# Performance work log

Measured on AMD Instinct MI355X. Metric: run time of the kernel, lower is better.

The kernel has to match this reference:

```python
import jax, jax.numpy as jnp
import numpy as np

N_HEADS = 4
M = 16            # n_points (neighbors kept per voxel)
DIST = 4          # manhattan distance threshold
D_MODEL = 128
D_FFN = 256
D_CHL = 64
GRID = 96         # spatial_shape per axis
LN_EPS = 1e-5
BN_EPS = 1e-3


def setup_inputs() -> dict:
    key = jax.random.key(0)
    ks = jax.random.split(key, 24)
    N = 8192
    w = lambda k, s: jax.random.normal(k, s, jnp.float32) * 0.02
    z = lambda d: jnp.zeros((d,), jnp.float32)
    o = lambda d: jnp.ones((d,), jnp.float32)
    return {
        "features": jax.random.normal(ks[0], (N, D_CHL), jnp.float32),
        "coords": jax.random.randint(ks[1], (N, 3), 0, GRID, jnp.int32),
        "pe_w1": w(ks[2], (3, D_MODEL // 2)), "pe_b1": z(D_MODEL // 2),
        "pe_w2": w(ks[3], (D_MODEL // 2, D_MODEL)), "pe_b2": z(D_MODEL),
        "in_w": w(ks[4], (D_CHL, D_MODEL)), "in_b": z(D_MODEL),
        "q_w": w(ks[5], (D_MODEL, D_MODEL)), "q_b": z(D_MODEL),
        "k_w": w(ks[6], (D_MODEL, D_MODEL)), "k_b": z(D_MODEL),
        "v_w": w(ks[7], (D_MODEL, D_MODEL)), "v_b": z(D_MODEL),
        "o_w": w(ks[8], (D_MODEL, D_MODEL)), "o_b": z(D_MODEL),
        "n1_g": o(D_MODEL), "n1_b": z(D_MODEL),
        "l1_w": w(ks[9], (D_MODEL, D_FFN)), "l1_b": z(D_FFN),
        "l2_w": w(ks[10], (D_FFN, D_MODEL)), "l2_b": z(D_MODEL),
        "n3_g": o(D_MODEL), "n3_b": z(D_MODEL),
        "fu_w": w(ks[11], (D_MODEL + D_CHL, D_CHL)), "fu_b": z(D_CHL),
        "bn_g": o(D_CHL), "bn_b": z(D_CHL),
    }


def _layernorm(x, g, b):
    mu = jnp.mean(x, -1, keepdims=True)
    var = jnp.mean(jnp.square(x - mu), -1, keepdims=True)
    return (x - mu) * jax.lax.rsqrt(var + LN_EPS) * g + b


def reference(features, coords, pe_w1, pe_b1, pe_w2, pe_b2, in_w, in_b,
              q_w, q_b, k_w, k_b, v_w, v_b, o_w, o_b, n1_g, n1_b,
              l1_w, l1_b, l2_w, l2_b, n3_g, n3_b, fu_w, fu_b, bn_g, bn_b):
    N = features.shape[0]
    hd = D_MODEL // N_HEADS
    ci = coords.astype(jnp.float32)
    # input projection + dynamic learnable positional encoding
    src = features @ in_w + in_b
    vc = ci / (GRID - 1.0)
    src = src + (jax.nn.relu(vc @ pe_w1 + pe_b1) @ pe_w2 + pe_b2)
    # pairwise manhattan distances; accumulate per coordinate to avoid [N,N,3]
    dist = jnp.zeros((N, N), jnp.float32)
    for d in range(3):
        dist = dist + jnp.abs(ci[:, d, None] - ci[None, :, d])
    dist = jnp.where(dist <= DIST, dist, jnp.inf)
    neg_top, idx = jax.lax.top_k(-dist, M)          # [N, M]
    valid = neg_top != -jnp.inf
    # gather neighbor features; invalid slots are zero (as in torch)
    nb = jnp.where(valid[:, :, None], src[jnp.where(valid, idx, 0)], 0.0)  # [N,M,D]
    # cross-attention: query is neighbor 0 (self). NOTE: faithful raw .view
    # reshape of [N,M,D] -> [N,H,M,hd] (interleaves neighbor/head axes as torch does)
    q = (nb[:, :1] @ q_w + q_b).reshape(N, N_HEADS, 1, hd)
    k = (nb @ k_w + k_b).reshape(N, N_HEADS, M, hd)
    v = (nb @ v_w + v_b).reshape(N, N_HEADS, M, hd)
    scores = jnp.einsum('nhqd,nhkd->nhqk', q, k) / jnp.sqrt(jnp.float32(D_MODEL))
    attn = jax.nn.softmax(scores, axis=-1)
    head_out = jnp.einsum('nhqk,nhkd->nhqd', attn, v).reshape(N, D_MODEL)
    out = head_out @ o_w + o_b
    tgt = _layernorm(src + out, n1_g, n1_b)
    # FFN
    tgt2 = jax.nn.relu(tgt @ l1_w + l1_b) @ l2_w + l2_b
    tgt = _layernorm(tgt + tgt2, n3_g, n3_b)
    # EnhancedFusion: concat -> linear -> batchnorm (train-mode stats) -> relu
    fused = jnp.concatenate([features, tgt], axis=1) @ fu_w + fu_b
    mu = jnp.mean(fused, 0)
    var = jnp.var(fused, 0)
    fused = (fused - mu) * jax.lax.rsqrt(var + BN_EPS) * bn_g + bn_b
    return jax.nn.relu(fused)
```

## Files before the change

kernel.cpp:

```cpp
#include <hip/hip_runtime.h>

#define DEVFN __device__ __forceinline__

DEVFN float relu(float x) { return x < 0.f ? 0.f : x; }

__global__ __launch_bounds__(256) void ka_pre_cst(
    const float* __restrict__ features, const int* __restrict__ coords,
    const float* __restrict__ pe_w1, const float* __restrict__ pe_b1,
    const float* __restrict__ pe_w2, const float* __restrict__ pe_b2,
    const float* __restrict__ in_w, const float* __restrict__ in_b,
    const float* __restrict__ q_w, const float* __restrict__ k_w,
    const float* __restrict__ v_w,
    float* __restrict__ src,
    float* __restrict__ qs, float* __restrict__ ks, float* __restrict__ vs,
    int* __restrict__ nbr, float* __restrict__ bnAcc, int N)
{
    __shared__ float sF[512];
    __shared__ float sH[512];
    __shared__ float S[1024];
    __shared__ int   sC[24];
    __shared__ int cnt[16];
    __shared__ int lst[16 * 64];
    __shared__ int outL[256];

    const int tid = threadIdx.x;
    const int nSrcBlocks = N / 8;

    if ((int)blockIdx.x >= nSrcBlocks) {
        const int nb = blockIdx.x - nSrcBlocks;
        const int q0 = nb * 16;
        if (nb == 0 && tid < 128) bnAcc[tid] = 0.f;
        if (tid < 16) cnt[tid] = 0;
        outL[tid] = -1;
        __syncthreads();
        int qx[16], qy[16], qz[16];
#pragma unroll
        for (int q = 0; q < 16; ++q) {
            qx[q] = coords[(q0 + q) * 3 + 0];
            qy[q] = coords[(q0 + q) * 3 + 1];
            qz[q] = coords[(q0 + q) * 3 + 2];
        }
        for (int cd = tid; cd < N; cd += 256) {
            int cx = coords[cd * 3 + 0];
            int cy = coords[cd * 3 + 1];
            int cz = coords[cd * 3 + 2];
#pragma unroll
            for (int q = 0; q < 16; ++q) {
                int dx = cx - qx[q]; dx = dx < 0 ? -dx : dx;
                int dy = cy - qy[q]; dy = dy < 0 ? -dy : dy;
                int dz = cz - qz[q]; dz = dz < 0 ? -dz : dz;
                int d = dx + dy + dz;
                if (d <= 4) {
                    int s = atomicAdd(&cnt[q], 1);
                    if (s < 64) lst[q * 64 + s] = (d << 13) | cd;
                }
            }
        }
        __syncthreads();
        {
            const int q = tid >> 4, t = tid & 15;
            int n = cnt[q]; if (n > 64) n = 64;
            for (int e = t; e < n; e += 16) {
                int key = lst[q * 64 + e];
                int rank = 0;
                for (int j = 0; j < n; ++j) rank += (lst[q * 64 + j] < key) ? 1 : 0;
                if (rank < 16) outL[q * 16 + rank] = key & 8191;
            }
        }
        __syncthreads();
        {
            const int q = tid >> 4, t = tid & 15;
            nbr[(q0 + q) * 16 + t] = outL[q * 16 + t];
        }
        return;
    }

    const int r0 = blockIdx.x * 8;
    if (tid < 24) sC[tid] = coords[r0 * 3 + tid];
    for (int i = tid; i < 512; i += 256) sF[i] = features[r0 * 64 + i];
    __syncthreads();
    for (int i = tid; i < 512; i += 256) {
        int r = i >> 6, t = i & 63;
        float v0 = sC[r * 3 + 0] * (1.f / 95.f);
        float v1 = sC[r * 3 + 1] * (1.f / 95.f);
        float v2 = sC[r * 3 + 2] * (1.f / 95.f);
        float h = v0 * pe_w1[t] + v1 * pe_w1[64 + t] + v2 * pe_w1[128 + t] + pe_b1[t];
        sH[i] = relu(h);
    }
    __syncthreads();
    const int c = tid & 127, rh = tid >> 7;
    {
        float acc[4];
        const float base = in_b[c] + pe_b2[c];
#pragma unroll
        for (int r = 0; r < 4; ++r) acc[r] = base;
        for (int j = 0; j < 64; ++j) {
            float w1 = in_w[j * 128 + c];
            float w2 = pe_w2[j * 128 + c];
#pragma unroll
            for (int r = 0; r < 4; ++r) {
                int rr = rh * 4 + r;
                acc[r] += sF[rr * 64 + j] * w1 + sH[rr * 64 + j] * w2;
            }
        }
#pragma unroll
        for (int r = 0; r < 4; ++r) {
            src[(r0 + rh * 4 + r) * 128 + c] = acc[r];
            S[(rh * 4 + r) * 128 + c] = acc[r];
        }
    }
    __syncthreads();
    {
        float aq[4], ak[4], av[4];
#pragma unroll
        for (int r = 0; r < 4; ++r) { aq[r] = 0.f; ak[r] = 0.f; av[r] = 0.f; }
        for (int k4 = 0; k4 < 32; ++k4) {
            float wq0 = q_w[(k4 * 4 + 0) * 128 + c];
            float wq1 = q_w[(k4 * 4 + 1) * 128 + c];
            float wq2 = q_w[(k4 * 4 + 2) * 128 + c];
            float wq3 = q_w[(k4 * 4 + 3) * 128 + c];
            float wk0 = k_w[(k4 * 4 + 0) * 128 + c];
            float wk1 = k_w[(k4 * 4 + 1) * 128 + c];
            float wk2 = k_w[(k4 * 4 + 2) * 128 + c];
            float wk3 = k_w[(k4 * 4 + 3) * 128 + c];
            float wv0 = v_w[(k4 * 4 + 0) * 128 + c];
            float wv1 = v_w[(k4 * 4 + 1) * 128 + c];
            float wv2 = v_w[(k4 * 4 + 2) * 128 + c];
            float wv3 = v_w[(k4 * 4 + 3) * 128 + c];
#pragma unroll
            for (int r = 0; r < 4; ++r) {
                float4 s = *(const float4*)(&S[(rh * 4 + r) * 128 + k4 * 4]);
                aq[r] += s.x * wq0 + s.y * wq1 + s.z * wq2 + s.w * wq3;
                ak[r] += s.x * wk0 + s.y * wk1 + s.z * wk2 + s.w * wk3;
                av[r] += s.x * wv0 + s.y * wv1 + s.z * wv2 + s.w * wv3;
            }
        }
#pragma unroll
        for (int r = 0; r < 4; ++r) {
            qs[(r0 + rh * 4 + r) * 128 + c] = aq[r];
            ks[(r0 + rh * 4 + r) * 128 + c] = ak[r];
            vs[(r0 + rh * 4 + r) * 128 + c] = av[r];
        }
    }
}

DEVFN void ln_rows8(float* Cb, const float* __restrict__ g,
                    const float* __restrict__ b, int tid)
{
    const int r = tid >> 5, l = tid & 31;
    float x[4]; float s = 0.f, s2 = 0.f;
#pragma unroll
    for (int i = 0; i < 4; ++i) {
        x[i] = Cb[r * 128 + l * 4 + i];
        s += x[i]; s2 += x[i] * x[i];
    }
#pragma unroll
    for (int o = 1; o < 32; o <<= 1) { s += __shfl_xor(s, o); s2 += __shfl_xor(s2, o); }
    float mu = s * (1.f / 128.f);
    float var = s2 * (1.f / 128.f) - mu * mu;
    float rstd = rsqrtf(var + 1e-5f);
#pragma unroll
    for (int i = 0; i < 4; ++i) {
        int cc = l * 4 + i;
        Cb[r * 128 + cc] = (x[i] - mu) * rstd * g[cc] + b[cc];
    }
}

__global__ __launch_bounds__(256) void k4_main_cst(
    const float* __restrict__ features, const float* __restrict__ src,
    const float* __restrict__ qs, const float* __restrict__ ks, const float* __restrict__ vs,
    const int* __restrict__ nbr,
    const float* __restrict__ q_b, const float* __restrict__ k_b,
    const float* __restrict__ v_b,
    const float* __restrict__ o_w, const float* __restrict__ o_b,
    const float* __restrict__ n1_g, const float* __restrict__ n1_b,
    const float* __restrict__ l1_w, const float* __restrict__ l1_b,
    const float* __restrict__ l2_w, const float* __restrict__ l2_b,
    const float* __restrict__ n3_g, const float* __restrict__ n3_b,
    const float* __restrict__ fu_w, const float* __restrict__ fu_b,
    float* __restrict__ fused, float* __restrict__ bnSum, float* __restrict__ bnSq)
{
    __shared__ float A[1024];
    __shared__ float Bt[1024];
    __shared__ float C[1024];
    __shared__ float Q[1024];
    __shared__ float H[2048];
    __shared__ float SC[512];
    __shared__ float F[512];
    __shared__ __align__(16) float bK[128], bV[128];
    __shared__ float bQ[128];
    __shared__ int idxL[128];
    const int tid = threadIdx.x;
    const int r0 = blockIdx.x * 8;

    for (int i = tid; i < 1024; i += 256) A[i] = src[r0 * 128 + i];
    for (int i = tid; i < 512; i += 256) F[i] = features[r0 * 64 + i];
    if (tid < 128) {
        idxL[tid] = nbr[r0 * 16 + tid];
        bQ[tid] = q_b[tid]; bK[tid] = k_b[tid]; bV[tid] = v_b[tid];
    }
    __syncthreads();
    for (int i = tid; i < 1024; i += 256) {
        int r = i >> 7, c = i & 127;
        int i0 = idxL[r * 16];
        Q[i] = (i0 < 0 ? 0.f : qs[i0 * 128 + c]) + bQ[c];
    }
    __syncthreads();

    const int ar = tid >> 5, ah = (tid >> 3) & 3, ag = tid & 7;
    {
#pragma unroll
        for (int jj = 0; jj < 2; ++jj) {
            int j = ag + jj * 8;
            int j4 = j >> 2, ch = j & 3;
            int id = idxL[ar * 16 + ah * 4 + j4];
            float s = 0.f;
#pragma unroll
            for (int c4 = 0; c4 < 8; ++c4) {
                float4 qv = *(const float4*)(&Q[ar * 128 + ah * 32 + c4 * 4]);
                float4 kb = *(const float4*)(&bK[ch * 32 + c4 * 4]);
                float4 kv = make_float4(0.f, 0.f, 0.f, 0.f);
                if (id >= 0) kv = *(const float4*)(ks + id * 128 + ch * 32 + c4 * 4);
                s += qv.x * (kv.x + kb.x) + qv.y * (kv.y + kb.y)
                   + qv.z * (kv.z + kb.z) + qv.w * (kv.w + kb.w);
            }
            SC[ar * 64 + ah * 16 + j] = s * 0.08838834764831845f;
        }
    }
    __syncthreads();

    {
        float p[16];
        float mx = -3.4e38f;
#pragma unroll
        for (int j = 0; j < 16; ++j) { p[j] = SC[ar * 64 + ah * 16 + j]; mx = fmaxf(mx, p[j]); }
        float sum = 0.f;
#pragma unroll
        for (int j = 0; j < 16; ++j) { p[j] = __expf(p[j] - mx); sum += p[j]; }
        float inv = 1.f / sum;
        float4 acc = make_float4(0.f, 0.f, 0.f, 0.f);
#pragma unroll
        for (int j = 0; j < 16; ++j) {
            int j4 = j >> 2, ch = j & 3;
            int id = idxL[ar * 16 + ah * 4 + j4];
            float4 vb = *(const float4*)(&bV[ch * 32 + ag * 4]);
            float4 vv = make_float4(0.f, 0.f, 0.f, 0.f);
            if (id >= 0) vv = *(const float4*)(vs + id * 128 + ch * 32 + ag * 4);
            float w = p[j] * inv;
            acc.x += w * (vv.x + vb.x); acc.y += w * (vv.y + vb.y);
            acc.z += w * (vv.z + vb.z); acc.w += w * (vv.w + vb.w);
        }
        *(float4*)(&Bt[ar * 128 + ah * 32 + ag * 4]) = acc;
    }
    __syncthreads();

    {
        const int c = tid & 127, rh = tid >> 7;
        float acc[4];
        const float ob = o_b[c];
#pragma unroll
        for (int r = 0; r < 4; ++r) acc[r] = ob;
        for (int k4 = 0; k4 < 32; ++k4) {
            float w0 = o_w[(k4 * 4 + 0) * 128 + c];
            float w1 = o_w[(k4 * 4 + 1) * 128 + c];
            float w2 = o_w[(k4 * 4 + 2) * 128 + c];
            float w3 = o_w[(k4 * 4 + 3) * 128 + c];
#pragma unroll
            for (int r = 0; r < 4; ++r) {
                float4 t = *(const float4*)(&Bt[(rh * 4 + r) * 128 + k4 * 4]);
                acc[r] += t.x * w0 + t.y * w1 + t.z * w2 + t.w * w3;
            }
        }
#pragma unroll
        for (int r = 0; r < 4; ++r) {
            int row = rh * 4 + r;
            C[row * 128 + c] = A[row * 128 + c] + acc[r];
        }
    }
    __syncthreads();
    ln_rows8(C, n1_g, n1_b, tid);
    __syncthreads();

    {
        const int f = tid;
        float acc[8];
#pragma unroll
        for (int r = 0; r < 8; ++r) acc[r] = 0.f;
        for (int k4 = 0; k4 < 32; ++k4) {
            float w0 = l1_w[(k4 * 4 + 0) * 256 + f];
            float w1 = l1_w[(k4 * 4 + 1) * 256 + f];
            float w2 = l1_w[(k4 * 4 + 2) * 256 + f];
            float w3 = l1_w[(k4 * 4 + 3) * 256 + f];
#pragma unroll
            for (int r = 0; r < 8; ++r) {
                float4 t = *(const float4*)(&C[r * 128 + k4 * 4]);
                acc[r] += t.x * w0 + t.y * w1 + t.z * w2 + t.w * w3;
            }
        }
        const float bb = l1_b[f];
#pragma unroll
        for (int r = 0; r < 8; ++r) H[r * 256 + f] = relu(acc[r] + bb);
    }
    __syncthreads();

    {
        const int c = tid & 127, rh = tid >> 7;
        float acc[4];
        const float lb = l2_b[c];
#pragma unroll
        for (int r = 0; r < 4; ++r) acc[r] = lb;
        for (int k4 = 0; k4 < 64; ++k4) {
            float w0 = l2_w[(k4 * 4 + 0) * 128 + c];
            float w1 = l2_w[(k4 * 4 + 1) * 128 + c];
            float w2 = l2_w[(k4 * 4 + 2) * 128 + c];
            float w3 = l2_w[(k4 * 4 + 3) * 128 + c];
#pragma unroll
            for (int r = 0; r < 4; ++r) {
                float4 t = *(const float4*)(&H[(rh * 4 + r) * 256 + k4 * 4]);
                acc[r] += t.x * w0 + t.y * w1 + t.z * w2 + t.w * w3;
            }
        }
#pragma unroll
        for (int r = 0; r < 4; ++r) {
            int row = rh * 4 + r;
            C[row * 128 + c] += acc[r];
        }
    }
    __syncthreads();
    ln_rows8(C, n3_g, n3_b, tid);
    __syncthreads();

    {
        const int c = tid & 63, rg = tid >> 6;
        float acc[2];
        const float fb = fu_b[c];
#pragma unroll
        for (int r = 0; r < 2; ++r) acc[r] = fb;
        for (int j4 = 0; j4 < 16; ++j4) {
            float w0 = fu_w[(j4 * 4 + 0) * 64 + c];
            float w1 = fu_w[(j4 * 4 + 1) * 64 + c];
            float w2 = fu_w[(j4 * 4 + 2) * 64 + c];
            float w3 = fu_w[(j4 * 4 + 3) * 64 + c];
#pragma unroll
            for (int r = 0; r < 2; ++r) {
                float4 t = *(const float4*)(&F[(rg * 2 + r) * 64 + j4 * 4]);
                acc[r] += t.x * w0 + t.y * w1 + t.z * w2 + t.w * w3;
            }
        }
        for (int j4 = 0; j4 < 32; ++j4) {
            float w0 = fu_w[(64 + j4 * 4 + 0) * 64 + c];
            float w1 = fu_w[(64 + j4 * 4 + 1) * 64 + c];
            float w2 = fu_w[(64 + j4 * 4 + 2) * 64 + c];
            float w3 = fu_w[(64 + j4 * 4 + 3) * 64 + c];
#pragma unroll
            for (int r = 0; r < 2; ++r) {
                float4 t = *(const float4*)(&C[(rg * 2 + r) * 128 + j4 * 4]);
                acc[r] += t.x * w0 + t.y * w1 + t.z * w2 + t.w * w3;
            }
        }
#pragma unroll
        for (int r = 0; r < 2; ++r) {
            int row = rg * 2 + r;
            float v = acc[r];
            fused[(r0 + row) * 64 + c] = v;
            H[row * 64 + c] = v;
        }
    }
    __syncthreads();
    if (tid < 64) {
        float s = 0.f, s2 = 0.f;
#pragma unroll
        for (int r = 0; r < 8; ++r) { float x = H[r * 64 + tid]; s += x; s2 += x * x; }
        atomicAdd(&bnSum[tid], s);
        atomicAdd(&bnSq[tid], s2);
    }
}

__global__ __launch_bounds__(256) void k5_bn_cst(
    const float* __restrict__ fused, const float* __restrict__ bnSum,
    const float* __restrict__ bnSq,
    const float* __restrict__ g, const float* __restrict__ b,
    float* __restrict__ out, int N)
{
    const int total = N * 64;
    const float invN = 1.f / (float)N;
    for (int i = blockIdx.x * 256 + threadIdx.x; i < total; i += gridDim.x * 256) {
        int c = i & 63;
        float mu = bnSum[c] * invN;
        float var = bnSq[c] * invN - mu * mu;
        float x = fused[i];
        float y = (x - mu) * rsqrtf(var + 1e-3f) * g[c] + b[c];
        out[i] = relu(y);
    }
}

extern "C" void kernel_launch(void* const* d_in, const int* in_sizes, int n_in,
                              void* d_out, int out_size, void* d_ws, size_t ws_size,
                              hipStream_t stream)
{
    const float* features = (const float*)d_in[0];
    const int*   coords   = (const int*)d_in[1];
    const float* pe_w1 = (const float*)d_in[2];
    const float* pe_b1 = (const float*)d_in[3];
    const float* pe_w2 = (const float*)d_in[4];
    const float* pe_b2 = (const float*)d_in[5];
    const float* in_w  = (const float*)d_in[6];
    const float* in_b  = (const float*)d_in[7];
    const float* q_w   = (const float*)d_in[8];
    const float* q_b   = (const float*)d_in[9];
    const float* k_w   = (const float*)d_in[10];
    const float* k_b   = (const float*)d_in[11];
    const float* v_w   = (const float*)d_in[12];
    const float* v_b   = (const float*)d_in[13];
    const float* o_w   = (const float*)d_in[14];
    const float* o_b   = (const float*)d_in[15];
    const float* n1_g  = (const float*)d_in[16];
    const float* n1_b  = (const float*)d_in[17];
    const float* l1_w  = (const float*)d_in[18];
    const float* l1_b  = (const float*)d_in[19];
    const float* l2_w  = (const float*)d_in[20];
    const float* l2_b  = (const float*)d_in[21];
    const float* n3_g  = (const float*)d_in[22];
    const float* n3_b  = (const float*)d_in[23];
    const float* fu_w  = (const float*)d_in[24];
    const float* fu_b  = (const float*)d_in[25];
    const float* bn_g  = (const float*)d_in[26];
    const float* bn_b  = (const float*)d_in[27];

    const int N = in_sizes[0] / 64;

    float* src   = (float*)d_ws;
    float* qs    = src + (size_t)N * 128;
    float* ks    = qs  + (size_t)N * 128;
    float* vs    = ks  + (size_t)N * 128;
    float* fused = vs  + (size_t)N * 128;
    int*   nbr    = (int*)(fused + (size_t)N * 64);
    float* bnSum  = (float*)(nbr + (size_t)N * 16);
    float* bnSq   = bnSum + 64;

    ka_pre_cst<<<N / 8 + N / 16, 256, 0, stream>>>(features, coords,
                                                   pe_w1, pe_b1, pe_w2, pe_b2,
                                                   in_w, in_b, q_w, k_w, v_w,
                                                   src, qs, ks, vs, nbr, bnSum, N);
    k4_main_cst<<<N / 8, 256, 0, stream>>>(features, src, qs, ks, vs, nbr,
                                           q_b, k_b, v_b, o_w, o_b, n1_g, n1_b,
                                           l1_w, l1_b, l2_w, l2_b, n3_g, n3_b,
                                           fu_w, fu_b, fused, bnSum, bnSq);
    k5_bn_cst<<<512, 256, 0, stream>>>(fused, bnSum, bnSq, bn_g, bn_b,
                                       (float*)d_out, N);
}
```

Baseline: 228.1 us.

## Split-K the o_proj and FFN2 GEMMs, interleave neighbor blocks, vectorize Q gather

The o_proj and l2 matmuls now split the reduction dimension across the two thread halves instead of splitting rows. Each thread covers all 8 rows, so every global weight load feeds twice as many FMAs, and the two partial sums are added afterwards through shared memory. The Q gather uses float4 loads with the bias read straight from global memory. In the pre kernel, the neighbor-search blocks are interleaved with the src blocks (every third block) so the heavy search work spreads across the GPU, and both kernels get a launch_bounds minimum-blocks hint. The cost is an extra shared-memory reduction pass and a sync, plus register pressure from the occupancy hint.

```diff
diff --git a/kernel.cpp b/kernel.cpp
--- a/kernel.cpp
+++ b/kernel.cpp
@@ -4,7 +4,7 @@
 
 DEVFN float relu(float x) { return x < 0.f ? 0.f : x; }
 
-__global__ __launch_bounds__(256) void ka_pre_cst(
+__global__ __launch_bounds__(256, 4) void ka_pre_cst(
     const float* __restrict__ features, const int* __restrict__ coords,
     const float* __restrict__ pe_w1, const float* __restrict__ pe_b1,
     const float* __restrict__ pe_w2, const float* __restrict__ pe_b2,
@@ -24,10 +24,11 @@
     __shared__ int outL[256];
 
     const int tid = threadIdx.x;
-    const int nSrcBlocks = N / 8;
-
-    if ((int)blockIdx.x >= nSrcBlocks) {
-        const int nb = blockIdx.x - nSrcBlocks;
+    const int bx = blockIdx.x;
+    const int role_nbr = (bx % 3) == 2;
+
+    if (role_nbr) {
+        const int nb = bx / 3;
         const int q0 = nb * 16;
         if (nb == 0 && tid < 128) bnAcc[tid] = 0.f;
         if (tid < 16) cnt[tid] = 0;
@@ -75,7 +76,8 @@
         return;
     }
 
-    const int r0 = blockIdx.x * 8;
+    const int sb = (bx / 3) * 2 + (bx % 3);
+    const int r0 = sb * 8;
     if (tid < 24) sC[tid] = coords[r0 * 3 + tid];
     for (int i = tid; i < 512; i += 256) sF[i] = features[r0 * 64 + i];
     __syncthreads();
@@ -166,7 +168,7 @@
     }
 }
 
-__global__ __launch_bounds__(256) void k4_main_cst(
+__global__ __launch_bounds__(256, 4) void k4_main_cst(
     const float* __restrict__ features, const float* __restrict__ src,
     const float* __restrict__ qs, const float* __restrict__ ks, const float* __restrict__ vs,
     const int* __restrict__ nbr,
@@ -188,7 +190,6 @@
     __shared__ float SC[512];
     __shared__ float F[512];
     __shared__ __align__(16) float bK[128], bV[128];
-    __shared__ float bQ[128];
     __shared__ int idxL[128];
     const int tid = threadIdx.x;
     const int r0 = blockIdx.x * 8;
@@ -197,13 +198,17 @@
     for (int i = tid; i < 512; i += 256) F[i] = features[r0 * 64 + i];
     if (tid < 128) {
         idxL[tid] = nbr[r0 * 16 + tid];
-        bQ[tid] = q_b[tid]; bK[tid] = k_b[tid]; bV[tid] = v_b[tid];
-    }
-    __syncthreads();
-    for (int i = tid; i < 1024; i += 256) {
-        int r = i >> 7, c = i & 127;
+        bK[tid] = k_b[tid]; bV[tid] = v_b[tid];
+    }
+    __syncthreads();
+    {
+        int r = tid >> 5, cg = tid & 31;
         int i0 = idxL[r * 16];
-        Q[i] = (i0 < 0 ? 0.f : qs[i0 * 128 + c]) + bQ[c];
+        float4 qv = make_float4(0.f, 0.f, 0.f, 0.f);
+        if (i0 >= 0) qv = *(const float4*)(qs + i0 * 128 + cg * 4);
+        float4 qb = *(const float4*)(q_b + cg * 4);
+        qv.x += qb.x; qv.y += qb.y; qv.z += qb.z; qv.w += qb.w;
+        *(float4*)(&Q[r * 128 + cg * 4]) = qv;
     }
     __syncthreads();
 
@@ -255,27 +260,29 @@
     __syncthreads();
 
     {
-        const int c = tid & 127, rh = tid >> 7;
-        float acc[4];
-        const float ob = o_b[c];
-#pragma unroll
-        for (int r = 0; r < 4; ++r) acc[r] = ob;
-        for (int k4 = 0; k4 < 32; ++k4) {
-            float w0 = o_w[(k4 * 4 + 0) * 128 + c];
-            float w1 = o_w[(k4 * 4 + 1) * 128 + c];
-            float w2 = o_w[(k4 * 4 + 2) * 128 + c];
-            float w3 = o_w[(k4 * 4 + 3) * 128 + c];
-#pragma unroll
-            for (int r = 0; r < 4; ++r) {
-                float4 t = *(const float4*)(&Bt[(rh * 4 + r) * 128 + k4 * 4]);
+        const int c = tid & 127, kh = tid >> 7;
+        float acc[8];
+#pragma unroll
+        for (int r = 0; r < 8; ++r) acc[r] = 0.f;
+        const float* wp = o_w + kh * 64 * 128 + c;
+        for (int k4 = 0; k4 < 16; ++k4) {
+            float w0 = wp[(k4 * 4 + 0) * 128];
+            float w1 = wp[(k4 * 4 + 1) * 128];
+            float w2 = wp[(k4 * 4 + 2) * 128];
+            float w3 = wp[(k4 * 4 + 3) * 128];
+#pragma unroll
+            for (int r = 0; r < 8; ++r) {
+                float4 t = *(const float4*)(&Bt[r * 128 + kh * 64 + k4 * 4]);
                 acc[r] += t.x * w0 + t.y * w1 + t.z * w2 + t.w * w3;
             }
         }
 #pragma unroll
-        for (int r = 0; r < 4; ++r) {
-            int row = rh * 4 + r;
-            C[row * 128 + c] = A[row * 128 + c] + acc[r];
-        }
+        for (int r = 0; r < 8; ++r) H[kh * 1024 + r * 128 + c] = acc[r];
+    }
+    __syncthreads();
+    for (int i = tid; i < 1024; i += 256) {
+        int c = i & 127;
+        C[i] = A[i] + o_b[c] + H[i] + H[1024 + i];
     }
     __syncthreads();
     ln_rows8(C, n1_g, n1_b, tid);
@@ -304,27 +311,30 @@
     __syncthreads();
 
     {
-        const int c = tid & 127, rh = tid >> 7;
-        float acc[4];
-        const float lb = l2_b[c];
-#pragma unroll
-        for (int r = 0; r < 4; ++r) acc[r] = lb;
-        for (int k4 = 0; k4 < 64; ++k4) {
-            float w0 = l2_w[(k4 * 4 + 0) * 128 + c];
-            float w1 = l2_w[(k4 * 4 + 1) * 128 + c];
-            float w2 = l2_w[(k4 * 4 + 2) * 128 + c];
-            float w3 = l2_w[(k4 * 4 + 3) * 128 + c];
-#pragma unroll
-            for (int r = 0; r < 4; ++r) {
-                float4 t = *(const float4*)(&H[(rh * 4 + r) * 256 + k4 * 4]);
+        const int c = tid & 127, kh = tid >> 7;
+        float acc[8];
+#pragma unroll
+        for (int r = 0; r < 8; ++r) acc[r] = 0.f;
+        const float* wp = l2_w + kh * 128 * 128 + c;
+        for (int k4 = 0; k4 < 32; ++k4) {
+            float w0 = wp[(k4 * 4 + 0) * 128];
+            float w1 = wp[(k4 * 4 + 1) * 128];
+            float w2 = wp[(k4 * 4 + 2) * 128];
+            float w3 = wp[(k4 * 4 + 3) * 128];
+#pragma unroll
+            for (int r = 0; r < 8; ++r) {
+                float4 t = *(const float4*)(&H[r * 256 + kh * 128 + k4 * 4]);
                 acc[r] += t.x * w0 + t.y * w1 + t.z * w2 + t.w * w3;
             }
         }
-#pragma unroll
-        for (int r = 0; r < 4; ++r) {
-            int row = rh * 4 + r;
-            C[row * 128 + c] += acc[r];
-        }
+        float* P = kh ? Bt : A;
+#pragma unroll
+        for (int r = 0; r < 8; ++r) P[r * 128 + c] = acc[r];
+    }
+    __syncthreads();
+    for (int i = tid; i < 1024; i += 256) {
+        int c = i & 127;
+        C[i] += l2_b[c] + A[i] + Bt[i];
     }
     __syncthreads();
     ln_rows8(C, n3_g, n3_b, tid);
```

After: 221.3 us. 3.0% less time.
